# Kernel tuning notes

Hardware: AMD Instinct MI355X
Metric: run time of the kernel (lower is better)

Reference implementation:

```python
import jax, jax.numpy as jnp
import numpy as np
import math

B, T, D = 16, 4096, 64   # batch, time steps, state_dim
K = 5                    # vmd_modes
M = 3                    # perm_dim
P = math.factorial(M)    # max_patterns = 6
FACT = [math.factorial(i) for i in range(M)]


def setup_inputs() -> dict:
    key = jax.random.key(0)
    return {"hidden_states": jax.random.normal(key, (B, T, D), dtype=jnp.float32)}


def reference(hidden_states):
    x = jnp.transpose(hidden_states, (0, 2, 1))  # [B, D, T]

    # ---- VMD: Gaussian-window frequency-domain filtering (T >= 2K branch) ----
    freqs = np.fft.fftfreq(T).astype(np.float32)          # [T]
    centers = ((np.arange(K) - K / 2.0) / K).astype(np.float32)  # [K]
    bandwidth = 1.0 / K
    mask = np.exp(-0.5 * (np.abs(freqs[None, :] - centers[:, None]) / bandwidth) ** 2)
    mask = jnp.asarray(mask, dtype=jnp.float32)           # [K, T]
    fx = jnp.fft.fft(x, axis=-1)                          # [B, D, T] complex
    modes = jnp.real(jnp.fft.ifft(fx[:, :, None, :] * mask[None, None], axis=-1))  # [B,D,K,T]

    # ---- TMPTM: sliding-window Lehmer codes + transition histogram ----
    W = T - M + 1
    widx = np.arange(W)[:, None] + np.arange(M)[None, :]  # [W, M] static gather indices
    wins = modes[..., widx]                               # [B, D, K, W, M]
    sort_idx = jnp.argsort(wins, axis=-1)                 # [B, D, K, W, M]
    ids = jnp.zeros(wins.shape[:-1], dtype=jnp.int32)
    for i in range(M - 1):  # small static loop over perm_dim
        smaller = jnp.sum(sort_idx[..., i:i + 1] > sort_idx[..., i + 1:], axis=-1)
        ids = ids + smaller.astype(jnp.int32) * FACT[M - 1 - i]

    curr = ids[..., :-1]  # [B, D, K, W-1]
    nxt = ids[..., 1:]
    base = (jnp.arange(B * D, dtype=jnp.int32) * (P * P)).reshape(B, D, 1, 1)
    lin = base + curr * P + nxt                           # per-(b,d) histogram offsets
    counts = jnp.bincount(lin.reshape(-1), length=B * D * P * P)
    tmptm = counts.reshape(B, D, P, P).astype(jnp.float32)
    row = jnp.sum(tmptm, axis=-1, keepdims=True)
    tmptm = tmptm / jnp.where(row == 0, 1.0, row)         # row-normalized transition matrix

    # ---- FMPTM: corrcoef of mode energies, strict upper triangle ----
    e = modes ** 2                                        # [B, D, K, T]
    c = e - jnp.mean(e, axis=-1, keepdims=True)
    cov = jnp.einsum('bdkt,bdlt->bdkl', c, c)             # scale cancels in corrcoef
    dstd = jnp.sqrt(jnp.diagonal(cov, axis1=-2, axis2=-1))  # [B, D, K]
    denom = dstd[..., :, None] * dstd[..., None, :]
    corr = jnp.where(denom > 0, cov / jnp.where(denom == 0, 1.0, denom), 0.0)
    corr = jnp.clip(corr, -1.0, 1.0)
    iu, ju = np.triu_indices(K, k=1)
    fm = corr[..., iu, ju]                                # [B, D, K*(K-1)/2]

    feats = jnp.concatenate([tmptm.reshape(B, D, P * P), fm], axis=-1)  # [B, D, 36+10]
    return feats.reshape(B, D * (P * P + iu.shape[0])).astype(jnp.float32)
```

## Files before the change

kernel.cpp:

```cpp
#include <hip/hip_runtime.h>
#include <math.h>


#define NTH 256
#define PHYS(i) ((i) + ((i) >> 4))

typedef _Float16 f16x8 __attribute__((ext_vector_type(8)));
typedef _Float16 f16x2 __attribute__((ext_vector_type(2)));

__device__ __forceinline__ float mask_f32(int k, int j) {
  float f = (float)((j < 2048) ? j : (j - 4096)) * (1.0f / 4096.0f);
  float c = ((float)k - 2.5f) / 5.0f;
  float df = fabsf(f - c);
  float q = df / 0.2f;
  return expf(-0.5f * (q * q));
}

__global__ void setup_k(const float* __restrict__ x, float* __restrict__ xT,
                        float2* __restrict__ Wt, float* __restrict__ Mdr, int n_trans) {
  __shared__ float tile[64][65];
  if ((int)blockIdx.x < n_trans) {
    int bb = blockIdx.x >> 6;
    int tt = blockIdx.x & 63;
    int lane = threadIdx.x & 63;
    int grp = threadIdx.x >> 6;
#pragma unroll
    for (int r = 0; r < 16; ++r) {
      int tl = grp + 4 * r;
      tile[tl][lane] = x[((size_t)bb * 4096 + tt * 64 + tl) * 64 + lane];
    }
    __syncthreads();
#pragma unroll
    for (int r = 0; r < 16; ++r) {
      int dl = grp + 4 * r;
      xT[((size_t)bb * 64 + dl) * 4096 + tt * 64 + lane] = tile[lane][dl];
    }
  } else {
    int j = (blockIdx.x - n_trans) * NTH + threadIdx.x;
    double ang = -(2.0 * 3.14159265358979323846 / 4096.0) * (double)j;
    double s, c;
    sincos(ang, &s, &c);
    Wt[j] = make_float2((float)c, (float)s);
    int jr = (int)(__brev((unsigned)j) >> 20);
    int jrn = (4096 - jr) & 4095;
#pragma unroll
    for (int k = 0; k < 3; ++k) {
      float m1 = mask_f32(k, jr);
      float m2 = mask_f32(k, jrn);
      Mdr[k * 4096 + j] = (float)(((double)m1 + (double)m2) * (0.5 / 4096.0));
    }
  }
}

template <int S, bool INV>
__device__ __forceinline__ void fft_stage(float* __restrict__ SRe, float* __restrict__ SIm,
                                          const float2* __restrict__ Wt, int tid) {
  const int LOG = 9 - 3 * S;
  const int sub = 1 << LOG;
#pragma unroll
  for (int gi = 0; gi < 2; ++gi) {
    const int g = tid + 256 * gi;
    const int b_hi = g >> LOG;
    const int b_lo = g & (sub - 1);
    const int base = b_hi * (sub << 3) + b_lo;
    int idx[8];
    float ar[8], ai[8];
#pragma unroll
    for (int q = 0; q < 8; ++q) {
      idx[q] = PHYS(base + q * sub);
      ar[q] = SRe[idx[q]];
      ai[q] = SIm[idx[q]];
    }
    float2 t1[4], t2[2], t3;
#pragma unroll
    for (int q = 0; q < 4; ++q) t1[q] = Wt[(b_lo + q * sub) << (3 * S)];
    t2[0] = Wt[b_lo << (3 * S + 1)];
    t2[1] = Wt[(b_lo + sub) << (3 * S + 1)];
    t3 = Wt[b_lo << (3 * S + 2)];
    if (!INV) {
#pragma unroll
      for (int q = 0; q < 4; ++q) {
        float ur = ar[q] - ar[q + 4], ui = ai[q] - ai[q + 4];
        ar[q] += ar[q + 4]; ai[q] += ai[q + 4];
        ar[q + 4] = ur * t1[q].x - ui * t1[q].y;
        ai[q + 4] = ur * t1[q].y + ui * t1[q].x;
      }
#pragma unroll
      for (int h = 0; h < 8; h += 4)
#pragma unroll
        for (int qq = 0; qq < 2; ++qq) {
          int q = h + qq;
          float ur = ar[q] - ar[q + 2], ui = ai[q] - ai[q + 2];
          ar[q] += ar[q + 2]; ai[q] += ai[q + 2];
          ar[q + 2] = ur * t2[qq].x - ui * t2[qq].y;
          ai[q + 2] = ur * t2[qq].y + ui * t2[qq].x;
        }
#pragma unroll
      for (int q = 0; q < 8; q += 2) {
        float ur = ar[q] - ar[q + 1], ui = ai[q] - ai[q + 1];
        ar[q] += ar[q + 1]; ai[q] += ai[q + 1];
        ar[q + 1] = ur * t3.x - ui * t3.y;
        ai[q + 1] = ur * t3.y + ui * t3.x;
      }
    } else {
#pragma unroll
      for (int q = 0; q < 8; q += 2) {
        float br = ar[q + 1] * t3.x + ai[q + 1] * t3.y;
        float bi = ai[q + 1] * t3.x - ar[q + 1] * t3.y;
        ar[q + 1] = ar[q] - br; ai[q + 1] = ai[q] - bi;
        ar[q] += br; ai[q] += bi;
      }
#pragma unroll
      for (int h = 0; h < 8; h += 4)
#pragma unroll
        for (int qq = 0; qq < 2; ++qq) {
          int q = h + qq;
          float br = ar[q + 2] * t2[qq].x + ai[q + 2] * t2[qq].y;
          float bi = ai[q + 2] * t2[qq].x - ar[q + 2] * t2[qq].y;
          ar[q + 2] = ar[q] - br; ai[q + 2] = ai[q] - bi;
          ar[q] += br; ai[q] += bi;
        }
#pragma unroll
      for (int q = 0; q < 4; ++q) {
        float br = ar[q + 4] * t1[q].x + ai[q + 4] * t1[q].y;
        float bi = ai[q + 4] * t1[q].x - ar[q + 4] * t1[q].y;
        ar[q + 4] = ar[q] - br; ai[q + 4] = ai[q] - bi;
        ar[q] += br; ai[q] += bi;
      }
    }
#pragma unroll
    for (int q = 0; q < 8; ++q) { SRe[idx[q]] = ar[q]; SIm[idx[q]] = ai[q]; }
  }
}

__device__ __forceinline__ void s3_fwd(float* ar, float* ai, const float2* __restrict__ Wt) {
  float2 t1[4];
#pragma unroll
  for (int q = 0; q < 4; ++q) t1[q] = Wt[q << 9];
  float2 t20 = Wt[0], t21 = Wt[1 << 10];
#pragma unroll
  for (int q = 0; q < 4; ++q) {
    float ur = ar[q] - ar[q + 4], ui = ai[q] - ai[q + 4];
    ar[q] += ar[q + 4]; ai[q] += ai[q + 4];
    ar[q + 4] = ur * t1[q].x - ui * t1[q].y;
    ai[q + 4] = ur * t1[q].y + ui * t1[q].x;
  }
#pragma unroll
  for (int h = 0; h < 8; h += 4)
#pragma unroll
    for (int qq = 0; qq < 2; ++qq) {
      int q = h + qq;
      float2 t = qq ? t21 : t20;
      float ur = ar[q] - ar[q + 2], ui = ai[q] - ai[q + 2];
      ar[q] += ar[q + 2]; ai[q] += ai[q + 2];
      ar[q + 2] = ur * t.x - ui * t.y;
      ai[q + 2] = ur * t.y + ui * t.x;
    }
#pragma unroll
  for (int q = 0; q < 8; q += 2) {
    float ur = ar[q] - ar[q + 1], ui = ai[q] - ai[q + 1];
    ar[q] += ar[q + 1]; ai[q] += ai[q + 1];
    ar[q + 1] = ur; ai[q + 1] = ui;
  }
}

__device__ __forceinline__ void s3_inv(float* ar, float* ai, const float2* __restrict__ Wt) {
  float2 t1[4];
#pragma unroll
  for (int q = 0; q < 4; ++q) t1[q] = Wt[q << 9];
  float2 t20 = Wt[0], t21 = Wt[1 << 10];
#pragma unroll
  for (int q = 0; q < 8; q += 2) {
    float br = ar[q + 1], bi = ai[q + 1];
    ar[q + 1] = ar[q] - br; ai[q + 1] = ai[q] - bi;
    ar[q] += br; ai[q] += bi;
  }
#pragma unroll
  for (int h = 0; h < 8; h += 4)
#pragma unroll
    for (int qq = 0; qq < 2; ++qq) {
      int q = h + qq;
      float2 t = qq ? t21 : t20;
      float br = ar[q + 2] * t.x + ai[q + 2] * t.y;
      float bi = ai[q + 2] * t.x - ar[q + 2] * t.y;
      ar[q + 2] = ar[q] - br; ai[q + 2] = ai[q] - bi;
      ar[q] += br; ai[q] += bi;
    }
#pragma unroll
  for (int q = 0; q < 4; ++q) {
    float br = ar[q + 4] * t1[q].x + ai[q + 4] * t1[q].y;
    float bi = ai[q + 4] * t1[q].x - ar[q + 4] * t1[q].y;
    ar[q + 4] = ar[q] - br; ai[q + 4] = ai[q] - bi;
    ar[q] += br; ai[q] += bi;
  }
}

__device__ __forceinline__ void corr_write(float* o, const float* st, int j) {
  const int k = (int)((440700928u >> (3 * j)) & 7u);
  const int l = (int)((611428561u >> (3 * j)) & 7u);
  const float Sk = st[k], Sl = st[l];
  const int offk = (k * (11 - k)) >> 1;
  const int offl = (l * (11 - l)) >> 1;
  const float Skl = st[5 + offk + (l - k)];
  const float Skk = st[5 + offk];
  const float Sll = st[5 + offl];
  const float invT = 1.0f / 4096.0f;
  float cov = Skl - Sk * Sl * invT;
  float vk = Skk - Sk * Sk * invT;
  float vl = Sll - Sl * Sl * invT;
  float dk = sqrtf(fmaxf(vk, 0.f)), dl = sqrtf(fmaxf(vl, 0.f));
  float den = dk * dl;
  float corr = den > 0.f ? cov / den : 0.f;
  o[36 + j] = fminf(1.f, fmaxf(-1.f, corr));
}

__global__ void __launch_bounds__(NTH, 2)
tf_main(const float* __restrict__ x,
        const float* __restrict__ xT, int use_xt,
        const float2* __restrict__ Wt,
        const float* __restrict__ Mdr,
        _Float16* __restrict__ E,
        float* __restrict__ out) {
  __shared__ float SRe[4352];
  __shared__ float SIm[4352];
  __shared__ unsigned char hist[NTH * 76];
  __shared__ float fnyb[2];

  const int tid = threadIdx.x;
  const int beta = blockIdx.x;
  const int b = beta >> 5;
  const int dA = (beta & 31) * 2;

  {
    unsigned int* hw = (unsigned int*)(hist + tid * 76);
#pragma unroll
    for (int i = 0; i < 19; ++i) hw[i] = 0u;
  }

  if (use_xt) {
    const float4* ra = (const float4*)(xT + (size_t)(b * 64 + dA) * 4096);
    const float4* rb = (const float4*)(xT + (size_t)(b * 64 + dA + 1) * 4096);
    for (int t4 = tid; t4 < 1024; t4 += NTH) {
      float4 va = ra[t4], vb = rb[t4];
      int t = t4 * 4;
      SRe[PHYS(t)] = va.x;     SIm[PHYS(t)] = vb.x;
      SRe[PHYS(t + 1)] = va.y; SIm[PHYS(t + 1)] = vb.y;
      SRe[PHYS(t + 2)] = va.z; SIm[PHYS(t + 2)] = vb.z;
      SRe[PHYS(t + 3)] = va.w; SIm[PHYS(t + 3)] = vb.w;
    }
  } else {
    const float2* xp = (const float2*)(x + (size_t)b * 4096 * 64 + dA);
    for (int t = tid; t < 4096; t += NTH) {
      float2 v = xp[(size_t)t * 32];
      SRe[PHYS(t)] = v.x;
      SIm[PHYS(t)] = v.y;
    }
  }
  __syncthreads();

  fft_stage<0, false>(SRe, SIm, Wt, tid); __syncthreads();
  fft_stage<1, false>(SRe, SIm, Wt, tid); __syncthreads();
  fft_stage<2, false>(SRe, SIm, Wt, tid); __syncthreads();

  float Fr[16], Fi[16];
#pragma unroll
  for (int j = 0; j < 16; ++j) {
    int p = PHYS(tid * 16 + j);
    Fr[j] = SRe[p]; Fi[j] = SIm[p];
  }
  s3_fwd(&Fr[0], &Fi[0], Wt);
  s3_fwd(&Fr[8], &Fi[8], Wt);
  if (tid == 0) { fnyb[0] = Fr[1]; fnyb[1] = Fi[1]; }

#pragma unroll
  for (int k = 0; k < 3; ++k) {
    __syncthreads();
#pragma unroll
    for (int h = 0; h < 2; ++h) {
      float Zr[8], Zi[8];
#pragma unroll
      for (int j = 0; j < 8; ++j) {
        float m = Mdr[k * 4096 + tid * 16 + h * 8 + j];
        Zr[j] = Fr[h * 8 + j] * m; Zi[j] = Fi[h * 8 + j] * m;
      }
      s3_inv(Zr, Zi, Wt);
#pragma unroll
      for (int j = 0; j < 8; ++j) {
        int p = PHYS(tid * 16 + h * 8 + j);
        SRe[p] = Zr[j]; SIm[p] = Zi[j];
      }
    }
    __syncthreads();
    fft_stage<2, true>(SRe, SIm, Wt, tid); __syncthreads();
    fft_stage<1, true>(SRe, SIm, Wt, tid); __syncthreads();
    fft_stage<0, true>(SRe, SIm, Wt, tid); __syncthreads();

    {
      const int t0 = tid * 16;
      float a0 = SRe[PHYS(t0)], a1 = SRe[PHYS(t0 + 1)];
      float c0 = SIm[PHYS(t0)], c1 = SIm[PHYS(t0 + 1)];
      alignas(16) _Float16 ehA[16], ehB[16];
      ehA[0] = (_Float16)(a0 * a0); ehA[1] = (_Float16)(a1 * a1);
      ehB[0] = (_Float16)(c0 * c0); ehB[1] = (_Float16)(c1 * c1);
      int pa = 0, pb = 0;
      unsigned char* myh = hist + tid * 76;

      float da = 0.f, db = 0.f;
      alignas(16) _Float16 ehA2[16], ehB2[16];
      float aq0 = 0.f, aq1 = 0.f, cq0 = 0.f, cq1 = 0.f;
      int pa2 = 0, pb2 = 0;
      if (k >= 1) {
        float m_mir = mask_f32(5 - k, 2048);
        float m_own = mask_f32(k, 2048);
        float dM = (float)(((double)m_mir - (double)m_own) * (1.0 / 4096.0));
        da = dM * fnyb[0];
        db = dM * fnyb[1];
        aq0 = a0 + da; aq1 = a1 - da;
        cq0 = c0 + db; cq1 = c1 - db;
        ehA2[0] = (_Float16)(aq0 * aq0); ehA2[1] = (_Float16)(aq1 * aq1);
        ehB2[0] = (_Float16)(cq0 * cq0); ehB2[1] = (_Float16)(cq1 * cq1);
      }

#pragma unroll
      for (int step = 0; step <= 16; ++step) {
        const int w = t0 + step;
        if (w < 4094) {
          float a2 = SRe[PHYS(w + 2)];
          float c2 = SIm[PHYS(w + 2)];
          if (step <= 13) {
            ehA[step + 2] = (_Float16)(a2 * a2);
            ehB[step + 2] = (_Float16)(c2 * c2);
          }
          int ia = (int)(a0 <= a1) | ((int)(a0 <= a2) << 1) | ((int)(a1 <= a2) << 2);
          int ca = (int)((537125u >> (3 * ia)) & 7u);
          int ib = (int)(c0 <= c1) | ((int)(c0 <= c2) << 1) | ((int)(c1 <= c2) << 2);
          int cb = (int)((537125u >> (3 * ib)) & 7u);
          if (step >= 1) { myh[pa * 6 + ca] += 1; myh[36 + pb * 6 + cb] += 1; }
          pa = ca; pb = cb;
          a0 = a1; a1 = a2;
          c0 = c1; c1 = c2;

          if (k >= 1) {
            const float sda = (step & 1) ? -da : da;
            const float sdb = (step & 1) ? -db : db;
            float aq2 = a2 + sda;
            float cq2 = c2 + sdb;
            if (step <= 13) {
              ehA2[step + 2] = (_Float16)(aq2 * aq2);
              ehB2[step + 2] = (_Float16)(cq2 * cq2);
            }
            int ia2 = (int)(aq0 <= aq1) | ((int)(aq0 <= aq2) << 1) | ((int)(aq1 <= aq2) << 2);
            int ca2 = (int)((537125u >> (3 * ia2)) & 7u);
            int ib2 = (int)(cq0 <= cq1) | ((int)(cq0 <= cq2) << 1) | ((int)(cq1 <= cq2) << 2);
            int cb2 = (int)((537125u >> (3 * ib2)) & 7u);
            if (step >= 1) { myh[pa2 * 6 + ca2] += 1; myh[36 + pb2 * 6 + cb2] += 1; }
            pa2 = ca2; pb2 = cb2;
            aq0 = aq1; aq1 = aq2;
            cq0 = cq1; cq1 = cq2;
          }
        }
      }
      f16x8* EA = (f16x8*)(E + ((size_t)(b * 64 + dA) * 5 + k) * 4096 + t0);
      f16x8* EB = (f16x8*)(E + ((size_t)(b * 64 + dA + 1) * 5 + k) * 4096 + t0);
      EA[0] = *(const f16x8*)&ehA[0]; EA[1] = *(const f16x8*)&ehA[8];
      EB[0] = *(const f16x8*)&ehB[0]; EB[1] = *(const f16x8*)&ehB[8];
      if (k >= 1) {
        const int mr = 5 - k;
        f16x8* EA2 = (f16x8*)(E + ((size_t)(b * 64 + dA) * 5 + mr) * 4096 + t0);
        f16x8* EB2 = (f16x8*)(E + ((size_t)(b * 64 + dA + 1) * 5 + mr) * 4096 + t0);
        EA2[0] = *(const f16x8*)&ehA2[0]; EA2[1] = *(const f16x8*)&ehA2[8];
        EB2[0] = *(const f16x8*)&ehB2[0]; EB2[1] = *(const f16x8*)&ehB2[8];
      }
    }
  }
  __syncthreads();

  unsigned int* histf = (unsigned int*)SRe;
  float* rowinv = SIm;
  if (tid < 72) {
    unsigned int s = 0;
    for (int i = 0; i < 256; ++i) s += (unsigned int)hist[i * 76 + tid];
    histf[tid] = s;
  }
  __syncthreads();
  if (tid < 12) {
    int base0 = (tid < 6 ? 0 : 36) + (tid % 6) * 6;
    float rs = (float)(histf[base0] + histf[base0 + 1] + histf[base0 + 2] +
                       histf[base0 + 3] + histf[base0 + 4] + histf[base0 + 5]);
    rowinv[tid] = rs > 0.f ? 1.0f / rs : 1.0f;
  }
  __syncthreads();

  float* oA = out + (size_t)(b * 64 + dA) * 46;
  float* oB = oA + 46;
  if (tid < 36) oA[tid] = (float)histf[tid] * rowinv[tid / 6];
  if (tid >= 64 && tid < 100) {
    int j = tid - 64;
    oB[j] = (float)histf[36 + j] * rowinv[6 + j / 6];
  }
}

__global__ void __launch_bounds__(NTH)
moments_k(const _Float16* __restrict__ E, float* __restrict__ out) {
  __shared__ float red[4][20];
  __shared__ float stats[20];
  const int bd = blockIdx.x;
  const int tid = threadIdx.x;
  const f16x2* Eb = (const f16x2*)(E + (size_t)bd * 5 * 4096);

  float acc[20];
#pragma unroll
  for (int j = 0; j < 20; ++j) acc[j] = 0.f;
  for (int i = 0; i < 8; ++i) {
    int t2 = tid + 256 * i;
    float ex[5], ey[5];
#pragma unroll
    for (int k = 0; k < 5; ++k) {
      f16x2 v = Eb[k * 2048 + t2];
      ex[k] = (float)v.x; ey[k] = (float)v.y;
    }
    int id5 = 5;
#pragma unroll
    for (int k = 0; k < 5; ++k) {
      acc[k] += ex[k] + ey[k];
#pragma unroll
      for (int l = k; l < 5; ++l) {
        acc[id5] += ex[k] * ex[l] + ey[k] * ey[l];
        ++id5;
      }
    }
  }
  const int lane = tid & 63, wv = tid >> 6;
#pragma unroll
  for (int j = 0; j < 20; ++j) {
    float v = acc[j];
    v += __shfl_down(v, 32, 64);
    v += __shfl_down(v, 16, 64);
    v += __shfl_down(v, 8, 64);
    v += __shfl_down(v, 4, 64);
    v += __shfl_down(v, 2, 64);
    v += __shfl_down(v, 1, 64);
    if (lane == 0) red[wv][j] = v;
  }
  __syncthreads();
  if (tid < 20) stats[tid] = red[0][tid] + red[1][tid] + red[2][tid] + red[3][tid];
  __syncthreads();
  if (tid < 10) corr_write(out + (size_t)bd * 46, stats, tid);
}

extern "C" void kernel_launch(void* const* d_in, const int* in_sizes, int n_in,
                              void* d_out, int out_size, void* d_ws, size_t ws_size,
                              hipStream_t stream) {
  (void)in_sizes; (void)n_in; (void)out_size;
  const float* x = (const float*)d_in[0];
  float* out = (float*)d_out;
  char* ws = (char*)d_ws;

  float2* Wt = (float2*)ws;
  float* Mdr = (float*)(ws + 32768);
  _Float16* E = (_Float16*)(ws + 131072);
  const size_t E_end = 131072 + (size_t)1024 * 5 * 4096 * 2;
  float* xT = (float*)(ws + E_end);
  int use_xt = (ws_size >= E_end + (size_t)16 * 64 * 4096 * 4) ? 1 : 0;
  int n_trans = use_xt ? 1024 : 0;

  setup_k<<<n_trans + 16, NTH, 0, stream>>>(x, xT, Wt, Mdr, n_trans);
  tf_main<<<512, NTH, 0, stream>>>(x, xT, use_xt, Wt, Mdr, E, out);
  moments_k<<<1024, NTH, 0, stream>>>(E, out);
}
```

Before: 121.5 us.

## Fuse mode-energy moments into main kernel, dropping fp16 energy buffer and third launch

Instead of writing squared mode values in fp16 to a global buffer and reducing them in a separate moments kernel, the main kernel keeps modes 0 and 1 (and their mirrors) in packed fp16 registers. It accumulates the 20 sum and cross-product moments while processing mode 2, then reduces them across the block and writes the correlation outputs. This removes about 40 MB of global writes and reads plus one kernel launch. In exchange it adds register pressure (80 extra fp16 registers and 40 accumulators) under launch bounds of 2 blocks per SM, which may cause spills. It also changes where fp16 rounding is applied to values before squaring.

```diff
diff --git a/kernel.cpp b/kernel.cpp
--- a/kernel.cpp
+++ b/kernel.cpp
@@ -5,8 +5,28 @@
 #define NTH 256
 #define PHYS(i) ((i) + ((i) >> 4))
 
-typedef _Float16 f16x8 __attribute__((ext_vector_type(8)));
 typedef _Float16 f16x2 __attribute__((ext_vector_type(2)));
+
+__device__ __forceinline__ void rset(f16x2* r, int j, float v) {
+  if (j & 1) r[j >> 1].y = (_Float16)v;
+  else       r[j >> 1].x = (_Float16)v;
+}
+__device__ __forceinline__ float rget(const f16x2* r, int j) {
+  return (j & 1) ? (float)r[j >> 1].y : (float)r[j >> 1].x;
+}
+
+__device__ __forceinline__ void madd5(float* acc, float m0, float m1, float m2,
+                                      float m3, float m4) {
+  float e[5];
+  e[0] = m0 * m0; e[1] = m1 * m1; e[2] = m2 * m2; e[3] = m3 * m3; e[4] = m4 * m4;
+  int id = 5;
+#pragma unroll
+  for (int a = 0; a < 5; ++a) {
+    acc[a] += e[a];
+#pragma unroll
+    for (int l = a; l < 5; ++l) { acc[id] += e[a] * e[l]; ++id; }
+  }
+}
 
 __device__ __forceinline__ float mask_f32(int k, int j) {
   float f = (float)((j < 2048) ? j : (j - 4096)) * (1.0f / 4096.0f);
@@ -219,7 +239,6 @@
         const float* __restrict__ xT, int use_xt,
         const float2* __restrict__ Wt,
         const float* __restrict__ Mdr,
-        _Float16* __restrict__ E,
         float* __restrict__ out) {
   __shared__ float SRe[4352];
   __shared__ float SIm[4352];
@@ -272,6 +291,10 @@
   s3_fwd(&Fr[8], &Fi[8], Wt);
   if (tid == 0) { fnyb[0] = Fr[1]; fnyb[1] = Fi[1]; }
 
+  f16x2 rA0[8], rB0[8], rA1[8], rB1[8];
+  float d4a = 0.f, d4b = 0.f;
+  float accA[20], accB[20];
+
 #pragma unroll
   for (int k = 0; k < 3; ++k) {
     __syncthreads();
@@ -299,14 +322,10 @@
       const int t0 = tid * 16;
       float a0 = SRe[PHYS(t0)], a1 = SRe[PHYS(t0 + 1)];
       float c0 = SIm[PHYS(t0)], c1 = SIm[PHYS(t0 + 1)];
-      alignas(16) _Float16 ehA[16], ehB[16];
-      ehA[0] = (_Float16)(a0 * a0); ehA[1] = (_Float16)(a1 * a1);
-      ehB[0] = (_Float16)(c0 * c0); ehB[1] = (_Float16)(c1 * c1);
       int pa = 0, pb = 0;
       unsigned char* myh = hist + tid * 76;
 
       float da = 0.f, db = 0.f;
-      alignas(16) _Float16 ehA2[16], ehB2[16];
       float aq0 = 0.f, aq1 = 0.f, cq0 = 0.f, cq1 = 0.f;
       int pa2 = 0, pb2 = 0;
       if (k >= 1) {
@@ -317,8 +336,22 @@
         db = dM * fnyb[1];
         aq0 = a0 + da; aq1 = a1 - da;
         cq0 = c0 + db; cq1 = c1 - db;
-        ehA2[0] = (_Float16)(aq0 * aq0); ehA2[1] = (_Float16)(aq1 * aq1);
-        ehB2[0] = (_Float16)(cq0 * cq0); ehB2[1] = (_Float16)(cq1 * cq1);
+      }
+      if (k == 1) { d4a = da; d4b = db; }
+
+      if (k == 0) {
+        rset(rA0, 0, a0); rset(rA0, 1, a1);
+        rset(rB0, 0, c0); rset(rB0, 1, c1);
+      } else if (k == 1) {
+        rset(rA1, 0, a0); rset(rA1, 1, a1);
+        rset(rB1, 0, c0); rset(rB1, 1, c1);
+      } else {
+#pragma unroll
+        for (int j = 0; j < 20; ++j) { accA[j] = 0.f; accB[j] = 0.f; }
+        madd5(accA, rget(rA0, 0), rget(rA1, 0), a0, a0 + da, rget(rA1, 0) + d4a);
+        madd5(accB, rget(rB0, 0), rget(rB1, 0), c0, c0 + db, rget(rB1, 0) + d4b);
+        madd5(accA, rget(rA0, 1), rget(rA1, 1), a1, a1 - da, rget(rA1, 1) - d4a);
+        madd5(accB, rget(rB0, 1), rget(rB1, 1), c1, c1 - db, rget(rB1, 1) - d4b);
       }
 
 #pragma unroll
@@ -327,9 +360,17 @@
         if (w < 4094) {
           float a2 = SRe[PHYS(w + 2)];
           float c2 = SIm[PHYS(w + 2)];
+          const float sg = (step & 1) ? -1.f : 1.f;
           if (step <= 13) {
-            ehA[step + 2] = (_Float16)(a2 * a2);
-            ehB[step + 2] = (_Float16)(c2 * c2);
+            const int j = step + 2;
+            if (k == 0) {
+              rset(rA0, j, a2); rset(rB0, j, c2);
+            } else if (k == 1) {
+              rset(rA1, j, a2); rset(rB1, j, c2);
+            } else {
+              madd5(accA, rget(rA0, j), rget(rA1, j), a2, a2 + sg * da, rget(rA1, j) + sg * d4a);
+              madd5(accB, rget(rB0, j), rget(rB1, j), c2, c2 + sg * db, rget(rB1, j) + sg * d4b);
+            }
           }
           int ia = (int)(a0 <= a1) | ((int)(a0 <= a2) << 1) | ((int)(a1 <= a2) << 2);
           int ca = (int)((537125u >> (3 * ia)) & 7u);
@@ -341,14 +382,10 @@
           c0 = c1; c1 = c2;
 
           if (k >= 1) {
-            const float sda = (step & 1) ? -da : da;
-            const float sdb = (step & 1) ? -db : db;
+            const float sda = sg * da;
+            const float sdb = sg * db;
             float aq2 = a2 + sda;
             float cq2 = c2 + sdb;
-            if (step <= 13) {
-              ehA2[step + 2] = (_Float16)(aq2 * aq2);
-              ehB2[step + 2] = (_Float16)(cq2 * cq2);
-            }
             int ia2 = (int)(aq0 <= aq1) | ((int)(aq0 <= aq2) << 1) | ((int)(aq1 <= aq2) << 2);
             int ca2 = (int)((537125u >> (3 * ia2)) & 7u);
             int ib2 = (int)(cq0 <= cq1) | ((int)(cq0 <= cq2) << 1) | ((int)(cq1 <= cq2) << 2);
@@ -360,23 +397,29 @@
           }
         }
       }
-      f16x8* EA = (f16x8*)(E + ((size_t)(b * 64 + dA) * 5 + k) * 4096 + t0);
-      f16x8* EB = (f16x8*)(E + ((size_t)(b * 64 + dA + 1) * 5 + k) * 4096 + t0);
-      EA[0] = *(const f16x8*)&ehA[0]; EA[1] = *(const f16x8*)&ehA[8];
-      EB[0] = *(const f16x8*)&ehB[0]; EB[1] = *(const f16x8*)&ehB[8];
-      if (k >= 1) {
-        const int mr = 5 - k;
-        f16x8* EA2 = (f16x8*)(E + ((size_t)(b * 64 + dA) * 5 + mr) * 4096 + t0);
-        f16x8* EB2 = (f16x8*)(E + ((size_t)(b * 64 + dA + 1) * 5 + mr) * 4096 + t0);
-        EA2[0] = *(const f16x8*)&ehA2[0]; EA2[1] = *(const f16x8*)&ehA2[8];
-        EB2[0] = *(const f16x8*)&ehB2[0]; EB2[1] = *(const f16x8*)&ehB2[8];
-      }
     }
   }
   __syncthreads();
 
+  float* red = SIm;
+  float* stats = SIm + 160;
+  float* rowinv = SIm + 200;
   unsigned int* histf = (unsigned int*)SRe;
-  float* rowinv = SIm;
+
+  const int lane = tid & 63, wv = tid >> 6;
+#pragma unroll
+  for (int j = 0; j < 40; ++j) {
+    float v = (j < 20) ? accA[j] : accB[j - 20];
+    v += __shfl_down(v, 32, 64);
+    v += __shfl_down(v, 16, 64);
+    v += __shfl_down(v, 8, 64);
+    v += __shfl_down(v, 4, 64);
+    v += __shfl_down(v, 2, 64);
+    v += __shfl_down(v, 1, 64);
+    if (lane == 0) red[wv * 40 + j] = v;
+  }
+  __syncthreads();
+  if (tid < 40) stats[tid] = red[tid] + red[40 + tid] + red[80 + tid] + red[120 + tid];
   if (tid < 72) {
     unsigned int s = 0;
     for (int i = 0; i < 256; ++i) s += (unsigned int)hist[i * 76 + tid];
@@ -398,54 +441,8 @@
     int j = tid - 64;
     oB[j] = (float)histf[36 + j] * rowinv[6 + j / 6];
   }
-}
-
-__global__ void __launch_bounds__(NTH)
-moments_k(const _Float16* __restrict__ E, float* __restrict__ out) {
-  __shared__ float red[4][20];
-  __shared__ float stats[20];
-  const int bd = blockIdx.x;
-  const int tid = threadIdx.x;
-  const f16x2* Eb = (const f16x2*)(E + (size_t)bd * 5 * 4096);
-
-  float acc[20];
-#pragma unroll
-  for (int j = 0; j < 20; ++j) acc[j] = 0.f;
-  for (int i = 0; i < 8; ++i) {
-    int t2 = tid + 256 * i;
-    float ex[5], ey[5];
-#pragma unroll
-    for (int k = 0; k < 5; ++k) {
-      f16x2 v = Eb[k * 2048 + t2];
-      ex[k] = (float)v.x; ey[k] = (float)v.y;
-    }
-    int id5 = 5;
-#pragma unroll
-    for (int k = 0; k < 5; ++k) {
-      acc[k] += ex[k] + ey[k];
-#pragma unroll
-      for (int l = k; l < 5; ++l) {
-        acc[id5] += ex[k] * ex[l] + ey[k] * ey[l];
-        ++id5;
-      }
-    }
-  }
-  const int lane = tid & 63, wv = tid >> 6;
-#pragma unroll
-  for (int j = 0; j < 20; ++j) {
-    float v = acc[j];
-    v += __shfl_down(v, 32, 64);
-    v += __shfl_down(v, 16, 64);
-    v += __shfl_down(v, 8, 64);
-    v += __shfl_down(v, 4, 64);
-    v += __shfl_down(v, 2, 64);
-    v += __shfl_down(v, 1, 64);
-    if (lane == 0) red[wv][j] = v;
-  }
-  __syncthreads();
-  if (tid < 20) stats[tid] = red[0][tid] + red[1][tid] + red[2][tid] + red[3][tid];
-  __syncthreads();
-  if (tid < 10) corr_write(out + (size_t)bd * 46, stats, tid);
+  if (tid >= 128 && tid < 138) corr_write(oA, stats, tid - 128);
+  if (tid >= 160 && tid < 170) corr_write(oB, stats + 20, tid - 160);
 }
 
 extern "C" void kernel_launch(void* const* d_in, const int* in_sizes, int n_in,
@@ -458,13 +455,10 @@
 
   float2* Wt = (float2*)ws;
   float* Mdr = (float*)(ws + 32768);
-  _Float16* E = (_Float16*)(ws + 131072);
-  const size_t E_end = 131072 + (size_t)1024 * 5 * 4096 * 2;
-  float* xT = (float*)(ws + E_end);
-  int use_xt = (ws_size >= E_end + (size_t)16 * 64 * 4096 * 4) ? 1 : 0;
+  float* xT = (float*)(ws + 131072);
+  int use_xt = (ws_size >= (size_t)131072 + (size_t)16 * 64 * 4096 * 4) ? 1 : 0;
   int n_trans = use_xt ? 1024 : 0;
 
   setup_k<<<n_trans + 16, NTH, 0, stream>>>(x, xT, Wt, Mdr, n_trans);
-  tf_main<<<512, NTH, 0, stream>>>(x, xT, use_xt, Wt, Mdr, E, out);
-  moments_k<<<1024, NTH, 0, stream>>>(E, out);
-}
+  tf_main<<<512, NTH, 0, stream>>>(x, xT, use_xt, Wt, Mdr, out);
+}
```

After: 116.5 us. -4.1%, faster.
